# Kernel tuning notes

Hardware: AMD Instinct MI355X
Metric: run time of the kernel (lower is better)

Reference implementation:

```python
import jax, jax.numpy as jnp
import numpy as np
import math

B, S, D = 2, 2048, 2048
H = 16
HD = D // H          # 128
LAT = 512            # latent_dim


def setup_inputs() -> dict:
    key = jax.random.key(0)
    ks = jax.random.split(key, 8)
    x = jax.random.normal(ks[0], (B, S, D), dtype=jnp.float32)
    freqs = jax.random.uniform(ks[1], (S, HD // 2), dtype=jnp.float32) * (2 * math.pi)
    # additive causal mask: 0 on/below diagonal, -1e9 above
    causal = jnp.tril(jnp.ones((S, S), dtype=bool))
    mask = jnp.where(causal, 0.0, -1e9).astype(jnp.float32)
    sc = 0.02
    Wq = jax.random.normal(ks[2], (D, H * HD), dtype=jnp.float32) * sc
    Wdown = jax.random.normal(ks[3], (D, LAT), dtype=jnp.float32) * sc
    Wkup = jax.random.normal(ks[4], (LAT, H * HD), dtype=jnp.float32) * sc
    Wvup = jax.random.normal(ks[5], (LAT, H * HD), dtype=jnp.float32) * sc
    Wo = jax.random.normal(ks[6], (D, D), dtype=jnp.float32) * sc
    return {"x": x, "freqs": freqs, "mask": mask,
            "Wq": Wq, "Wdown": Wdown, "Wkup": Wkup, "Wvup": Wvup, "Wo": Wo}


def _apply_rope(t, cos, sin):
    # t: [B, S, H, HD]; cos/sin: [1, S, 1, HD//2]
    tp = t.reshape(t.shape[:-1] + (HD // 2, 2))
    t0, t1 = tp[..., 0], tp[..., 1]
    rot = jnp.stack([t0 * cos - t1 * sin, t0 * sin + t1 * cos], axis=-1)
    return rot.reshape(t.shape)


def reference(x, freqs, mask, Wq, Wdown, Wkup, Wvup, Wo):
    b, s, d = x.shape
    Q = (x @ Wq).reshape(b, s, H, HD)
    c_kv = x @ Wdown                       # [B, S, LAT] low-rank latent
    K = (c_kv @ Wkup).reshape(b, s, H, HD)
    V = (c_kv @ Wvup).reshape(b, s, H, HD)
    cos = jnp.cos(freqs)[None, :, None, :]
    sin = jnp.sin(freqs)[None, :, None, :]
    Q = _apply_rope(Q, cos, sin)
    K = _apply_rope(K, cos, sin)
    scores = jnp.einsum('bqhd,bkhd->bhqk', Q, K) / math.sqrt(HD)
    scores = scores + mask                 # [S,S] broadcast over [B,H,S,S]
    probs = jax.nn.softmax(scores, axis=-1)
    attn = jnp.einsum('bhqk,bkhd->bqhd', probs, V).reshape(b, s, d)
    return attn @ Wo
```

## Files before the change

### kernel.cpp

```cpp
#include <hip/hip_runtime.h>
#include <hip/hip_bf16.h>
#include <math.h>

typedef __hip_bfloat16 bf16;
typedef __attribute__((ext_vector_type(8))) short short8;
typedef __attribute__((ext_vector_type(4))) float f32x4;
typedef __attribute__((ext_vector_type(16))) float f32x16;

static constexpr int BB   = 2;
static constexpr int SS   = 2048;
static constexpr int DD   = 2048;
static constexpr int NH   = 16;
static constexpr int HDD  = 128;
static constexpr int LATD = 512;
static constexpr int MR   = BB * SS;
static constexpr int QRS  = DD + LATD;

#if __has_builtin(__builtin_amdgcn_exp2f)
#define EXP2F(x) __builtin_amdgcn_exp2f(x)
#else
#define EXP2F(x) exp2f(x)
#endif

__device__ __forceinline__ void async_cp16(const void* g, void* l) {
    __builtin_amdgcn_global_load_lds(
        (const __attribute__((address_space(1))) void*)g,
        (__attribute__((address_space(3))) void*)l, 16, 0, 0);
}

__device__ __forceinline__ unsigned short bf_bits(bf16 v) {
    union { bf16 b; unsigned short u; } cv; cv.b = v; return cv.u;
}

__global__ __launch_bounds__(256) void prep(
    const float* __restrict__ x, bf16* __restrict__ xb,
    const float* __restrict__ Wq, const float* __restrict__ Wdown,
    const float* __restrict__ Wkup, const float* __restrict__ Wvup,
    bf16* __restrict__ WqdT, bf16* __restrict__ WkvT) {
    __shared__ float tile[32][33];
    const int blk = blockIdx.x, tid = threadIdx.x;
    if (blk < 8192) {
        const int i = blk * 256 + tid;
        float4 v = ((const float4*)x)[i];
        ushort4 o;
        o.x = bf_bits(__float2bfloat16(v.x));
        o.y = bf_bits(__float2bfloat16(v.y));
        o.z = bf_bits(__float2bfloat16(v.z));
        o.w = bf_bits(__float2bfloat16(v.w));
        ((ushort4*)xb)[i] = o;
        return;
    }
    const float* in; bf16* out; int rows, cols, bx, by;
    if (blk < 12288) {
        const int l = blk - 8192;  in = Wq;    out = WqdT;
        rows = DD;   cols = DD;    bx = l & 63; by = l >> 6;
    } else if (blk < 13312) {
        const int l = blk - 12288; in = Wdown; out = WqdT + (size_t)DD * DD;
        rows = DD;   cols = LATD;  bx = l & 15; by = l >> 4;
    } else if (blk < 14336) {
        const int l = blk - 13312; in = Wkup;  out = WkvT;
        rows = LATD; cols = DD;    bx = l & 63; by = l >> 6;
    } else {
        const int l = blk - 14336; in = Wvup;  out = WkvT + (size_t)DD * LATD;
        rows = LATD; cols = DD;    bx = l & 63; by = l >> 6;
    }
    const int tx = tid & 31, ty = tid >> 5;
    const int c0 = bx * 32, r0 = by * 32;
    for (int i = 0; i < 32; i += 8)
        tile[ty + i][tx] = in[(size_t)(r0 + ty + i) * cols + c0 + tx];
    __syncthreads();
    for (int i = 0; i < 32; i += 8)
        out[(size_t)(c0 + ty + i) * rows + r0 + tx] =
            __float2bfloat16(tile[tx][ty + i]);
}

template <bool OUT_F32>
__global__ __launch_bounds__(256) void gemm_bt(
    const bf16* __restrict__ A, const bf16* __restrict__ Bt,
    void* __restrict__ Cout, int M, int N, int K, int lda, int ldb, int ldc) {
    __shared__ bf16 As[2][128 * 32];
    __shared__ bf16 Bs[2][128 * 32];
    const int tid  = threadIdx.x;
    const int lane = tid & 63, wave = tid >> 6;
    const int quad = lane >> 4, l16 = lane & 15;
    const int row0 = blockIdx.y * 128, col0 = blockIdx.x * 128;
    const int wm = (wave >> 1) * 64, wn = (wave & 1) * 64;
    const int srow = lane >> 2;
    const int scol = (lane & 3) * 8;

    f32x4 acc[4][4];
    for (int i = 0; i < 4; ++i)
        for (int j = 0; j < 4; ++j)
            for (int r = 0; r < 4; ++r) acc[i][j][r] = 0.f;

    auto stage = [&](int k0, int bufi) {
        for (int c = 0; c < 2; ++c) {
            const int chunk = wave * 2 + c;
            const int r = chunk * 16 + srow;
            async_cp16(A  + (size_t)(row0 + r) * lda + k0 + scol, &As[bufi][chunk * 512]);
            async_cp16(Bt + (size_t)(col0 + r) * ldb + k0 + scol, &Bs[bufi][chunk * 512]);
        }
    };

    const int nk = K / 32;
    stage(0, 0);
    for (int ki = 0; ki < nk; ++ki) {
        __syncthreads();
        if (ki + 1 < nk) stage((ki + 1) * 32, (ki + 1) & 1);
        const int bi = ki & 1;
        short8 af[4], bfr[4];
        for (int t = 0; t < 4; ++t) {
            af[t]  = *(const short8*)&As[bi][(wm + t * 16 + l16) * 32 + quad * 8];
            bfr[t] = *(const short8*)&Bs[bi][(wn + t * 16 + l16) * 32 + quad * 8];
        }
        for (int i = 0; i < 4; ++i)
            for (int j = 0; j < 4; ++j)
                acc[i][j] = __builtin_amdgcn_mfma_f32_16x16x32_bf16(
                    af[i], bfr[j], acc[i][j], 0, 0, 0);
    }

    const int rbase = row0 + wm + quad * 4;
    const int cbase = col0 + wn + l16;
    if (OUT_F32) {
        float* C = (float*)Cout;
        for (int i = 0; i < 4; ++i)
            for (int j = 0; j < 4; ++j)
                for (int r = 0; r < 4; ++r)
                    C[(size_t)(rbase + i * 16 + r) * ldc + cbase + j * 16] = acc[i][j][r];
    } else {
        bf16* C = (bf16*)Cout;
        for (int i = 0; i < 4; ++i)
            for (int j = 0; j < 4; ++j)
                for (int r = 0; r < 4; ++r)
                    C[(size_t)(rbase + i * 16 + r) * ldc + cbase + j * 16] =
                        __float2bfloat16(acc[i][j][r]);
    }
}

__global__ __launch_bounds__(256) void tvrope(
    bf16* __restrict__ KV, bf16* __restrict__ VT,
    const float* __restrict__ freqs,
    const float* __restrict__ Wo, bf16* __restrict__ WoT) {
    __shared__ __align__(16) char sm[64 * 74 * 2];
    const int blk = blockIdx.x, tid = threadIdx.x;
    if (blk < 2048) {
        bf16 (*t)[74] = (bf16(*)[74])sm;
        const int bx = blk & 31, byy = (blk >> 5) & 1, bh = blk >> 6;
        const int s0 = bx * 64, d0 = byy * 64;
        const int b = bh >> 4, h = bh & 15;
        const bf16* src = KV + (size_t)b * SS * 4096 + 2048 + h * 128 + d0;
        for (int p = 0; p < 2; ++p) {
            const int s = p * 32 + (tid >> 3), dc = (tid & 7) * 8;
            short8 v = *(const short8*)(src + (size_t)(s0 + s) * 4096 + dc);
            const bf16* ve = (const bf16*)&v;
            for (int e = 0; e < 8; ++e) t[s][dc + e] = ve[e];
        }
        __syncthreads();
        bf16* dst = VT + ((size_t)bh * HDD + d0) * SS + s0;
        for (int p = 0; p < 2; ++p) {
            const int d = p * 32 + (tid >> 3), g = tid & 7;
            short8 v; bf16* ve = (bf16*)&v;
            for (int e = 0; e < 8; ++e) ve[e] = t[g * 8 + e][d];
            const int gp = g ^ (d & 7);
            *(short8*)(dst + (size_t)d * SS + gp * 8) = v;
        }
        return;
    }
    if (blk < 6144) {
        const int idx = (blk - 2048) * 256 + tid;
        const int pg  = idx & 15;
        const int h   = (idx >> 4) & (NH - 1);
        const int tok = idx >> 8;
        const int s   = tok & (SS - 1);
        const float4 f = *(const float4*)&freqs[s * 64 + pg * 4];
        const float fr[4] = {f.x, f.y, f.z, f.w};
        bf16* kp = KV + (size_t)tok * 4096 + h * HDD + pg * 8;
        short8 v = *(const short8*)kp;
        const bf16* ve = (const bf16*)&v;
        short8 o; bf16* oe = (bf16*)&o;
        for (int i = 0; i < 4; ++i) {
            const float cs = __cosf(fr[i]), sn = __sinf(fr[i]);
            const float t0 = __bfloat162float(ve[2 * i]);
            const float t1 = __bfloat162float(ve[2 * i + 1]);
            oe[2 * i]     = __float2bfloat16(t0 * cs - t1 * sn);
            oe[2 * i + 1] = __float2bfloat16(t0 * sn + t1 * cs);
        }
        *(short8*)kp = o;
        return;
    }
    {
        float (*tile)[33] = (float(*)[33])sm;
        const int l = blk - 6144;
        const int bx = l & 63, by = l >> 6;
        const int tx = tid & 31, ty = tid >> 5;
        const int c0 = bx * 32, r0 = by * 32;
        for (int i = 0; i < 32; i += 8)
            tile[ty + i][tx] = Wo[(size_t)(r0 + ty + i) * DD + c0 + tx];
        __syncthreads();
        for (int i = 0; i < 32; i += 8)
            WoT[(size_t)(c0 + ty + i) * DD + r0 + tx] =
                __float2bfloat16(tile[tx][ty + i]);
    }
}

__global__ __launch_bounds__(256, 2) void flash_attn(
    const bf16* __restrict__ QC, const bf16* __restrict__ KV,
    const bf16* __restrict__ VTg, const float* __restrict__ freqs,
    bf16* __restrict__ O) {
    const int j = blockIdx.x;
    const int bh = (j >> 3) & 31, q3 = j & 7;
    const int qt = (j & 256) ? q3 : 15 - q3;
    const int h = bh & (NH - 1), b = bh >> 4;
    const int q0 = qt * 128;
    const int tid = threadIdx.x, lane = tid & 63, wave = tid >> 6;
    const int l32 = lane & 31, hi = lane >> 5;

    __shared__ __align__(16) char smem[66048];
    bf16*  KsB  = (bf16*)smem;
    bf16*  VtB  = (bf16*)(smem + 32768);
    float* RedS = (float*)(smem + 65536);

    const bf16* Kb  = KV  + (size_t)b * SS * 4096 + h * HDD;
    const bf16* VTb = VTg + (size_t)bh * HDD * SS;

    const float QS = 0.08838834764831845f * 1.4426950408889634f;
    const int qrow = q0 + wave * 32 + l32;
    short8 qf[8];
    {
        const bf16* qp = QC + (size_t)(b * SS + qrow) * QRS + h * HDD;
#pragma unroll
        for (int dk = 0; dk < 8; ++dk) {
            short8 v = *(const short8*)(qp + dk * 16 + hi * 8);
            const float4 f = *(const float4*)&freqs[(size_t)qrow * 64 + dk * 8 + hi * 4];
            const float fr[4] = {f.x, f.y, f.z, f.w};
            const bf16* ve = (const bf16*)&v;
            bf16* oe = (bf16*)&qf[dk];
#pragma unroll
            for (int i2 = 0; i2 < 4; ++i2) {
                const float cs = __cosf(fr[i2]), sn = __sinf(fr[i2]);
                const float t0 = __bfloat162float(ve[2 * i2]);
                const float t1 = __bfloat162float(ve[2 * i2 + 1]);
                oe[2 * i2]     = __float2bfloat16((t0 * cs - t1 * sn) * QS);
                oe[2 * i2 + 1] = __float2bfloat16((t0 * sn + t1 * cs) * QS);
            }
        }
    }

    auto stage = [&](int kt, int bufi) {
        const int k0 = kt * 64;
#pragma unroll
        for (int ii = 0; ii < 4; ++ii) {
            const int i = wave * 4 + ii;
            const int krow = 4 * i + (lane >> 4);
            const int csrc = (lane & 15) ^ (krow & 7);
            async_cp16(Kb + (size_t)(k0 + krow) * 4096 + csrc * 8,
                       KsB + bufi * 8192 + i * 512);
            const int d = 8 * i + (lane >> 3);
            async_cp16(VTb + (size_t)d * SS + k0 + (lane & 7) * 8,
                       VtB + bufi * 8192 + i * 512);
        }
    };

    f32x16 accO[4];
#pragma unroll
    for (int d = 0; d < 4; ++d)
#pragma unroll
        for (int r = 0; r < 16; ++r) accO[d][r] = 0.f;
    float m_r = -1e30f, l_r = 0.f;

    const int ktMax = 2 * qt + 1;
    const int qwb = q0 + wave * 32;

    stage(0, 0);
    for (int kt = 0; kt <= ktMax; ++kt) {
        const int k0 = kt * 64;
        __syncthreads();
        if (kt < ktMax) stage(kt + 1, (kt + 1) & 1);
        const int bi = kt & 1;

        if (k0 > qwb + 31) continue;

        f32x16 st[2];
#pragma unroll
        for (int t = 0; t < 2; ++t)
#pragma unroll
            for (int r = 0; r < 16; ++r) st[t][r] = 0.f;
        __builtin_amdgcn_s_setprio(1);
#pragma unroll
        for (int dk = 0; dk < 8; ++dk)
#pragma unroll
            for (int t = 0; t < 2; ++t) {
                const int rd = t * 32 + l32;
                short8 kf = *(const short8*)
                    &KsB[bi * 8192 + rd * 128 + ((((dk << 1) | hi) ^ (rd & 7)) << 3)];
                st[t] = __builtin_amdgcn_mfma_f32_32x32x16_bf16(
                    kf, qf[dk], st[t], 0, 0, 0);
            }
        __builtin_amdgcn_s_setprio(0);

        float p[32];
#pragma unroll
        for (int t = 0; t < 2; ++t)
#pragma unroll
            for (int r = 0; r < 16; ++r) p[t * 16 + r] = st[t][r];

        if (k0 + 63 > qwb) {
#pragma unroll
            for (int t = 0; t < 2; ++t)
#pragma unroll
                for (int r = 0; r < 16; ++r) {
                    const int kv = k0 + t * 32 + (r & 3) + 8 * (r >> 2) + 4 * hi;
                    if (kv > qrow) p[t * 16 + r] = -1e30f;
                }
        }

        float mt[16];
#pragma unroll
        for (int n = 0; n < 16; ++n) mt[n] = fmaxf(p[n], p[n + 16]);
#pragma unroll
        for (int n = 0; n < 8; ++n) mt[n] = fmaxf(mt[n], mt[n + 8]);
#pragma unroll
        for (int n = 0; n < 4; ++n) mt[n] = fmaxf(mt[n], mt[n + 4]);
        float mx = fmaxf(fmaxf(mt[0], mt[1]), fmaxf(mt[2], mt[3]));
        const float rmax = fmaxf(mx, __shfl_xor(mx, 32));

        const bool grow = rmax > m_r + 8.f;
        if (__any(grow)) {
            const float mnew = fmaxf(m_r, rmax);
            const float alpha = EXP2F(m_r - mnew);
            m_r = mnew;
            l_r *= alpha;
            RedS[wave * 32 + l32] = alpha;
            __builtin_amdgcn_s_waitcnt(0xc07f);
#pragma unroll
            for (int r = 0; r < 16; ++r) {
                const float av = RedS[wave * 32 + ((r & 3) + 8 * (r >> 2) + 4 * hi)];
#pragma unroll
                for (int d = 0; d < 4; ++d) accO[d][r] *= av;
            }
        }

#pragma unroll
        for (int r = 0; r < 32; ++r) p[r] = EXP2F(p[r] - m_r);
        float sa[16];
#pragma unroll
        for (int n = 0; n < 16; ++n) sa[n] = p[n] + p[n + 16];
#pragma unroll
        for (int n = 0; n < 8; ++n) sa[n] += sa[n + 8];
#pragma unroll
        for (int n = 0; n < 4; ++n) sa[n] += sa[n + 4];
        float ps = (sa[0] + sa[1]) + (sa[2] + sa[3]);
        l_r += ps + __shfl_xor(ps, 32);

        unsigned int pk[16];
#pragma unroll
        for (int n = 0; n < 16; ++n) {
            const unsigned int lo = bf_bits(__float2bfloat16(p[2 * n]));
            const unsigned int hl = bf_bits(__float2bfloat16(p[2 * n + 1]));
            pk[n] = lo | (hl << 16);
        }

#pragma unroll
        for (int m = 0; m < 4; ++m) {
            const int A0 = 4 * m;
            const unsigned int op0 = __shfl_xor(pk[A0 + 0], 32);
            const unsigned int op1 = __shfl_xor(pk[A0 + 1], 32);
            const unsigned int op2 = __shfl_xor(pk[A0 + 2], 32);
            const unsigned int op3 = __shfl_xor(pk[A0 + 3], 32);
            union { unsigned int w[4]; short8 s; } fr;
            fr.w[0] = hi ? op2 : pk[A0 + 0];
            fr.w[1] = hi ? op3 : pk[A0 + 1];
            fr.w[2] = hi ? pk[A0 + 2] : op0;
            fr.w[3] = hi ? pk[A0 + 3] : op1;
            __builtin_amdgcn_s_setprio(1);
#pragma unroll
            for (int db = 0; db < 4; ++db) {
                const int d = db * 32 + l32;
                short8 vf = *(const short8*)
                    &VtB[bi * 8192 + d * 64 + ((((m << 1) | hi) ^ (d & 7)) << 3)];
                accO[db] = __builtin_amdgcn_mfma_f32_32x32x16_bf16(
                    fr.s, vf, accO[db], 0, 0, 0);
            }
            __builtin_amdgcn_s_setprio(0);
        }
    }

    const float invl = 1.f / l_r;
    RedS[wave * 32 + l32] = invl;
    __builtin_amdgcn_s_waitcnt(0xc07f);
    bf16* Ob = O + (size_t)b * SS * DD + h * HDD;
#pragma unroll
    for (int r = 0; r < 16; ++r) {
        const int row = (r & 3) + 8 * (r >> 2) + 4 * hi;
        const float iv = RedS[wave * 32 + row];
        const size_t ro = (size_t)(q0 + wave * 32 + row) * DD;
#pragma unroll
        for (int db = 0; db < 4; ++db)
            Ob[ro + db * 32 + l32] = __float2bfloat16(accO[db][r] * iv);
    }
}

extern "C" void kernel_launch(void* const* d_in, const int* in_sizes, int n_in,
                              void* d_out, int out_size, void* d_ws, size_t ws_size,
                              hipStream_t stream) {
    (void)in_sizes; (void)n_in; (void)out_size; (void)ws_size;
    const float* x     = (const float*)d_in[0];
    const float* freqs = (const float*)d_in[1];
    const float* Wq    = (const float*)d_in[3];
    const float* Wdown = (const float*)d_in[4];
    const float* Wkup  = (const float*)d_in[5];
    const float* Wvup  = (const float*)d_in[6];
    const float* Wo    = (const float*)d_in[7];
    float* out = (float*)d_out;

    char* ws = (char*)d_ws;
    size_t off = 0;
    auto take = [&](size_t bytes) -> void* {
        void* p = ws + off;
        off += (bytes + 255) & ~(size_t)255;
        return p;
    };
    bf16* xb    = (bf16*)take((size_t)MR * DD * 2);
    bf16* WqdT  = (bf16*)take((size_t)QRS * DD * 2);
    bf16* WkvT  = (bf16*)take((size_t)2 * DD * LATD * 2);
    bf16* QC    = (bf16*)take((size_t)MR * QRS * 2);
    bf16* KVb   = (bf16*)take((size_t)MR * 2 * DD * 2);
    bf16* VTg   = (bf16*)take((size_t)BB * NH * HDD * SS * 2);
    bf16* attn  = xb;
    bf16* WoT   = WqdT;

    prep<<<15360, 256, 0, stream>>>(x, xb, Wq, Wdown, Wkup, Wvup, WqdT, WkvT);

    gemm_bt<false><<<dim3(QRS / 128, MR / 128), 256, 0, stream>>>(
        xb, WqdT, QC, MR, QRS, DD, DD, DD, QRS);
    gemm_bt<false><<<dim3(2 * DD / 128, MR / 128), 256, 0, stream>>>(
        QC + DD, WkvT, KVb, MR, 2 * DD, LATD, QRS, LATD, 2 * DD);

    tvrope<<<10240, 256, 0, stream>>>(KVb, VTg, freqs, Wo, WoT);

    flash_attn<<<512, 256, 0, stream>>>(QC, KVb, VTg, freqs, attn);

    gemm_bt<true><<<dim3(DD / 128, MR / 128), 256, 0, stream>>>(
        attn, WoT, out, MR, DD, DD, DD, DD, DD);
}
```

Before: 347.3 us.

## Process two 32-row query sub-tiles per wave with 128-thread attention blocks

The flash attention kernel now runs 2 waves per block instead of 4, and each wave handles 64 query rows as two 32-row sub-tiles. Every K and V fragment read from LDS feeds two MFMAs, which halves LDS reads per FLOP. Each wave also issues twice as many staging copies. In exchange register pressure roughly doubles for accumulators and Q fragments, launch bounds drop to one block of 128 threads, and there are fewer waves per CU to hide latency. The causal early-exit is now coarser (64-row granularity), so some masked work is computed.

Measured after the change: 423.9 us. +22.0%, slower.

```diff
diff --git a/kernel.cpp b/kernel.cpp
--- a/kernel.cpp
+++ b/kernel.cpp
@@ -203,7 +203,7 @@
     }
 }
 
-__global__ __launch_bounds__(256, 2) void flash_attn(
+__global__ __launch_bounds__(128, 1) void flash_attn(
     const bf16* __restrict__ QC, const bf16* __restrict__ KV,
     const bf16* __restrict__ VTg, const float* __restrict__ freqs,
     bf16* __restrict__ O) {
@@ -224,17 +224,19 @@
     const bf16* VTb = VTg + (size_t)bh * HDD * SS;
 
     const float QS = 0.08838834764831845f * 1.4426950408889634f;
-    const int qrow = q0 + wave * 32 + l32;
-    short8 qf[8];
-    {
-        const bf16* qp = QC + (size_t)(b * SS + qrow) * QRS + h * HDD;
+    const int qwb = q0 + wave * 64;
+    short8 qf[2][8];
+#pragma unroll
+    for (int s = 0; s < 2; ++s) {
+        const int qr = qwb + s * 32 + l32;
+        const bf16* qp = QC + (size_t)(b * SS + qr) * QRS + h * HDD;
 #pragma unroll
         for (int dk = 0; dk < 8; ++dk) {
             short8 v = *(const short8*)(qp + dk * 16 + hi * 8);
-            const float4 f = *(const float4*)&freqs[(size_t)qrow * 64 + dk * 8 + hi * 4];
+            const float4 f = *(const float4*)&freqs[(size_t)qr * 64 + dk * 8 + hi * 4];
             const float fr[4] = {f.x, f.y, f.z, f.w};
             const bf16* ve = (const bf16*)&v;
-            bf16* oe = (bf16*)&qf[dk];
+            bf16* oe = (bf16*)&qf[s][dk];
 #pragma unroll
             for (int i2 = 0; i2 < 4; ++i2) {
                 const float cs = __cosf(fr[i2]), sn = __sinf(fr[i2]);
@@ -249,8 +251,8 @@
     auto stage = [&](int kt, int bufi) {
         const int k0 = kt * 64;
 #pragma unroll
-        for (int ii = 0; ii < 4; ++ii) {
-            const int i = wave * 4 + ii;
+        for (int ii = 0; ii < 8; ++ii) {
+            const int i = wave * 8 + ii;
             const int krow = 4 * i + (lane >> 4);
             const int csrc = (lane & 15) ^ (krow & 7);
             async_cp16(Kb + (size_t)(k0 + krow) * 4096 + csrc * 8,
@@ -261,15 +263,16 @@
         }
     };
 
-    f32x16 accO[4];
-#pragma unroll
-    for (int d = 0; d < 4; ++d)
-#pragma unroll
-        for (int r = 0; r < 16; ++r) accO[d][r] = 0.f;
-    float m_r = -1e30f, l_r = 0.f;
+    f32x16 accO[2][4];
+#pragma unroll
+    for (int s = 0; s < 2; ++s)
+#pragma unroll
+        for (int d = 0; d < 4; ++d)
+#pragma unroll
+            for (int r = 0; r < 16; ++r) accO[s][d][r] = 0.f;
+    float m_r[2] = {-1e30f, -1e30f}, l_r[2] = {0.f, 0.f};
 
     const int ktMax = 2 * qt + 1;
-    const int qwb = q0 + wave * 32;
 
     stage(0, 0);
     for (int kt = 0; kt <= ktMax; ++kt) {
@@ -278,13 +281,15 @@
         if (kt < ktMax) stage(kt + 1, (kt + 1) & 1);
         const int bi = kt & 1;
 
-        if (k0 > qwb + 31) continue;
-
-        f32x16 st[2];
-#pragma unroll
-        for (int t = 0; t < 2; ++t)
-#pragma unroll
-            for (int r = 0; r < 16; ++r) st[t][r] = 0.f;
+        if (k0 > qwb + 63) continue;
+
+        f32x16 st[2][2];
+#pragma unroll
+        for (int s = 0; s < 2; ++s)
+#pragma unroll
+            for (int t = 0; t < 2; ++t)
+#pragma unroll
+                for (int r = 0; r < 16; ++r) st[s][t][r] = 0.f;
         __builtin_amdgcn_s_setprio(1);
 #pragma unroll
         for (int dk = 0; dk < 8; ++dk)
@@ -293,111 +298,126 @@
                 const int rd = t * 32 + l32;
                 short8 kf = *(const short8*)
                     &KsB[bi * 8192 + rd * 128 + ((((dk << 1) | hi) ^ (rd & 7)) << 3)];
-                st[t] = __builtin_amdgcn_mfma_f32_32x32x16_bf16(
-                    kf, qf[dk], st[t], 0, 0, 0);
+                st[0][t] = __builtin_amdgcn_mfma_f32_32x32x16_bf16(
+                    kf, qf[0][dk], st[0][t], 0, 0, 0);
+                st[1][t] = __builtin_amdgcn_mfma_f32_32x32x16_bf16(
+                    kf, qf[1][dk], st[1][t], 0, 0, 0);
             }
         __builtin_amdgcn_s_setprio(0);
 
-        float p[32];
-#pragma unroll
-        for (int t = 0; t < 2; ++t)
-#pragma unroll
-            for (int r = 0; r < 16; ++r) p[t * 16 + r] = st[t][r];
-
-        if (k0 + 63 > qwb) {
+        unsigned int pk[2][16];
+        const bool boundary = (k0 + 63 > qwb);
+#pragma unroll
+        for (int s = 0; s < 2; ++s) {
+            float p[32];
 #pragma unroll
             for (int t = 0; t < 2; ++t)
 #pragma unroll
+                for (int r = 0; r < 16; ++r) p[t * 16 + r] = st[s][t][r];
+
+            if (boundary) {
+                const int qr = qwb + s * 32 + l32;
+#pragma unroll
+                for (int t = 0; t < 2; ++t)
+#pragma unroll
+                    for (int r = 0; r < 16; ++r) {
+                        const int kv = k0 + t * 32 + (r & 3) + 8 * (r >> 2) + 4 * hi;
+                        if (kv > qr) p[t * 16 + r] = -1e30f;
+                    }
+            }
+
+            float mt[16];
+#pragma unroll
+            for (int n = 0; n < 16; ++n) mt[n] = fmaxf(p[n], p[n + 16]);
+#pragma unroll
+            for (int n = 0; n < 8; ++n) mt[n] = fmaxf(mt[n], mt[n + 8]);
+#pragma unroll
+            for (int n = 0; n < 4; ++n) mt[n] = fmaxf(mt[n], mt[n + 4]);
+            float mx = fmaxf(fmaxf(mt[0], mt[1]), fmaxf(mt[2], mt[3]));
+            const float rmax = fmaxf(mx, __shfl_xor(mx, 32));
+
+            const bool grow = rmax > m_r[s] + 8.f;
+            if (__any(grow)) {
+                const float mnew = fmaxf(m_r[s], rmax);
+                const float alpha = EXP2F(m_r[s] - mnew);
+                m_r[s] = mnew;
+                l_r[s] *= alpha;
+                RedS[(wave * 2 + s) * 32 + l32] = alpha;
+                __builtin_amdgcn_s_waitcnt(0xc07f);
+#pragma unroll
                 for (int r = 0; r < 16; ++r) {
-                    const int kv = k0 + t * 32 + (r & 3) + 8 * (r >> 2) + 4 * hi;
-                    if (kv > qrow) p[t * 16 + r] = -1e30f;
+                    const float av =
+                        RedS[(wave * 2 + s) * 32 + ((r & 3) + 8 * (r >> 2) + 4 * hi)];
+#pragma unroll
+                    for (int d = 0; d < 4; ++d) accO[s][d][r] *= av;
                 }
-        }
-
-        float mt[16];
-#pragma unroll
-        for (int n = 0; n < 16; ++n) mt[n] = fmaxf(p[n], p[n + 16]);
-#pragma unroll
-        for (int n = 0; n < 8; ++n) mt[n] = fmaxf(mt[n], mt[n + 8]);
-#pragma unroll
-        for (int n = 0; n < 4; ++n) mt[n] = fmaxf(mt[n], mt[n + 4]);
-        float mx = fmaxf(fmaxf(mt[0], mt[1]), fmaxf(mt[2], mt[3]));
-        const float rmax = fmaxf(mx, __shfl_xor(mx, 32));
-
-        const bool grow = rmax > m_r + 8.f;
-        if (__any(grow)) {
-            const float mnew = fmaxf(m_r, rmax);
-            const float alpha = EXP2F(m_r - mnew);
-            m_r = mnew;
-            l_r *= alpha;
-            RedS[wave * 32 + l32] = alpha;
-            __builtin_amdgcn_s_waitcnt(0xc07f);
-#pragma unroll
-            for (int r = 0; r < 16; ++r) {
-                const float av = RedS[wave * 32 + ((r & 3) + 8 * (r >> 2) + 4 * hi)];
-#pragma unroll
-                for (int d = 0; d < 4; ++d) accO[d][r] *= av;
-            }
-        }
-
-#pragma unroll
-        for (int r = 0; r < 32; ++r) p[r] = EXP2F(p[r] - m_r);
-        float sa[16];
-#pragma unroll
-        for (int n = 0; n < 16; ++n) sa[n] = p[n] + p[n + 16];
-#pragma unroll
-        for (int n = 0; n < 8; ++n) sa[n] += sa[n + 8];
-#pragma unroll
-        for (int n = 0; n < 4; ++n) sa[n] += sa[n + 4];
-        float ps = (sa[0] + sa[1]) + (sa[2] + sa[3]);
-        l_r += ps + __shfl_xor(ps, 32);
-
-        unsigned int pk[16];
-#pragma unroll
-        for (int n = 0; n < 16; ++n) {
-            const unsigned int lo = bf_bits(__float2bfloat16(p[2 * n]));
-            const unsigned int hl = bf_bits(__float2bfloat16(p[2 * n + 1]));
-            pk[n] = lo | (hl << 16);
+            }
+
+#pragma unroll
+            for (int r = 0; r < 32; ++r) p[r] = EXP2F(p[r] - m_r[s]);
+            float sa[16];
+#pragma unroll
+            for (int n = 0; n < 16; ++n) sa[n] = p[n] + p[n + 16];
+#pragma unroll
+            for (int n = 0; n < 8; ++n) sa[n] += sa[n + 8];
+#pragma unroll
+            for (int n = 0; n < 4; ++n) sa[n] += sa[n + 4];
+            float ps = (sa[0] + sa[1]) + (sa[2] + sa[3]);
+            l_r[s] += ps + __shfl_xor(ps, 32);
+
+#pragma unroll
+            for (int n = 0; n < 16; ++n) {
+                const unsigned int lo = bf_bits(__float2bfloat16(p[2 * n]));
+                const unsigned int hl = bf_bits(__float2bfloat16(p[2 * n + 1]));
+                pk[s][n] = lo | (hl << 16);
+            }
         }
 
 #pragma unroll
         for (int m = 0; m < 4; ++m) {
             const int A0 = 4 * m;
-            const unsigned int op0 = __shfl_xor(pk[A0 + 0], 32);
-            const unsigned int op1 = __shfl_xor(pk[A0 + 1], 32);
-            const unsigned int op2 = __shfl_xor(pk[A0 + 2], 32);
-            const unsigned int op3 = __shfl_xor(pk[A0 + 3], 32);
-            union { unsigned int w[4]; short8 s; } fr;
-            fr.w[0] = hi ? op2 : pk[A0 + 0];
-            fr.w[1] = hi ? op3 : pk[A0 + 1];
-            fr.w[2] = hi ? pk[A0 + 2] : op0;
-            fr.w[3] = hi ? pk[A0 + 3] : op1;
+            union { unsigned int w[4]; short8 s8; } fr[2];
+#pragma unroll
+            for (int s = 0; s < 2; ++s) {
+                const unsigned int u = hi ? pk[s][A0 + 0] : pk[s][A0 + 2];
+                const unsigned int v = hi ? pk[s][A0 + 1] : pk[s][A0 + 3];
+                const unsigned int su = __shfl_xor(u, 32);
+                const unsigned int sv = __shfl_xor(v, 32);
+                fr[s].w[0] = hi ? su : pk[s][A0 + 0];
+                fr[s].w[1] = hi ? sv : pk[s][A0 + 1];
+                fr[s].w[2] = hi ? pk[s][A0 + 2] : su;
+                fr[s].w[3] = hi ? pk[s][A0 + 3] : sv;
+            }
             __builtin_amdgcn_s_setprio(1);
 #pragma unroll
             for (int db = 0; db < 4; ++db) {
                 const int d = db * 32 + l32;
                 short8 vf = *(const short8*)
                     &VtB[bi * 8192 + d * 64 + ((((m << 1) | hi) ^ (d & 7)) << 3)];
-                accO[db] = __builtin_amdgcn_mfma_f32_32x32x16_bf16(
-                    fr.s, vf, accO[db], 0, 0, 0);
+                accO[0][db] = __builtin_amdgcn_mfma_f32_32x32x16_bf16(
+                    fr[0].s8, vf, accO[0][db], 0, 0, 0);
+                accO[1][db] = __builtin_amdgcn_mfma_f32_32x32x16_bf16(
+                    fr[1].s8, vf, accO[1][db], 0, 0, 0);
             }
             __builtin_amdgcn_s_setprio(0);
         }
     }
 
-    const float invl = 1.f / l_r;
-    RedS[wave * 32 + l32] = invl;
+    RedS[(wave * 2 + 0) * 32 + l32] = 1.f / l_r[0];
+    RedS[(wave * 2 + 1) * 32 + l32] = 1.f / l_r[1];
     __builtin_amdgcn_s_waitcnt(0xc07f);
     bf16* Ob = O + (size_t)b * SS * DD + h * HDD;
 #pragma unroll
-    for (int r = 0; r < 16; ++r) {
-        const int row = (r & 3) + 8 * (r >> 2) + 4 * hi;
-        const float iv = RedS[wave * 32 + row];
-        const size_t ro = (size_t)(q0 + wave * 32 + row) * DD;
-#pragma unroll
-        for (int db = 0; db < 4; ++db)
-            Ob[ro + db * 32 + l32] = __float2bfloat16(accO[db][r] * iv);
-    }
+    for (int s = 0; s < 2; ++s)
+#pragma unroll
+        for (int r = 0; r < 16; ++r) {
+            const int row = (r & 3) + 8 * (r >> 2) + 4 * hi;
+            const float iv = RedS[(wave * 2 + s) * 32 + row];
+            const size_t ro = (size_t)(qwb + s * 32 + row) * DD;
+#pragma unroll
+            for (int db = 0; db < 4; ++db)
+                Ob[ro + db * 32 + l32] = __float2bfloat16(accO[s][db][r] * iv);
+        }
 }
 
 extern "C" void kernel_launch(void* const* d_in, const int* in_sizes, int n_in,
@@ -438,7 +458,7 @@
 
     tvrope<<<10240, 256, 0, stream>>>(KVb, VTg, freqs, Wo, WoT);
 
-    flash_attn<<<512, 256, 0, stream>>>(QC, KVb, VTg, freqs, attn);
+    flash_attn<<<512, 128, 0, stream>>>(QC, KVb, VTg, freqs, attn);
 
     gemm_bt<true><<<dim3(DD / 128, MR / 128), 256, 0, stream>>>(
         attn, WoT, out, MR, DD, DD, DD, DD, DD);
```

## Replace GEMM with 256x256-tile, 4-stage pipelined, swizzled LDS kernel

Applied to the files above, without the earlier changes.

Swaps the 128x128 double-buffered GEMM for a 512-thread kernel computing 256x256 output tiles with a 4-deep async-copy ring buffer in 128KB of LDS. It XOR-swizzles LDS columns to avoid bank conflicts, remaps workgroup IDs into banded tiles for L2 locality, and splits each k-step into two MFMA halves with s_setprio around loads. The aim is more data reuse per byte loaded and better overlap of memory with MFMA. In exchange each CU holds one workgroup, so small grids (e.g. 160 or 256 blocks on 256 CUs) may leave the machine underfilled.

Result: slower. 366.3 us (+5.5%).

```diff
diff --git a/kernel.cpp b/kernel.cpp
--- a/kernel.cpp
+++ b/kernel.cpp
@@ -75,65 +75,120 @@
 }
 
 template <bool OUT_F32>
-__global__ __launch_bounds__(256) void gemm_bt(
+__global__ __launch_bounds__(512) void gemm256(
     const bf16* __restrict__ A, const bf16* __restrict__ Bt,
     void* __restrict__ Cout, int M, int N, int K, int lda, int ldb, int ldc) {
-    __shared__ bf16 As[2][128 * 32];
-    __shared__ bf16 Bs[2][128 * 32];
+    __shared__ __align__(16) char smem[131072];
     const int tid  = threadIdx.x;
     const int lane = tid & 63, wave = tid >> 6;
     const int quad = lane >> 4, l16 = lane & 15;
-    const int row0 = blockIdx.y * 128, col0 = blockIdx.x * 128;
-    const int wm = (wave >> 1) * 64, wn = (wave & 1) * 64;
-    const int srow = lane >> 2;
-    const int scol = (lane & 3) * 8;
-
-    f32x4 acc[4][4];
-    for (int i = 0; i < 4; ++i)
-        for (int j = 0; j < 4; ++j)
-            for (int r = 0; r < 4; ++r) acc[i][j][r] = 0.f;
-
-    auto stage = [&](int k0, int bufi) {
-        for (int c = 0; c < 2; ++c) {
-            const int chunk = wave * 2 + c;
-            const int r = chunk * 16 + srow;
-            async_cp16(A  + (size_t)(row0 + r) * lda + k0 + scol, &As[bufi][chunk * 512]);
-            async_cp16(Bt + (size_t)(col0 + r) * ldb + k0 + scol, &Bs[bufi][chunk * 512]);
-        }
+    const int wm = wave >> 2, wn = wave & 3;
+
+    const int nx = N >> 8, ny = M >> 8;
+    const int nwg = nx * ny;
+    const int wg   = ((blockIdx.x & 7) * (nwg >> 3)) + (blockIdx.x >> 3);
+    const int idx  = wg % (nx << 2);
+    const int band = wg / (nx << 2);
+    const int bcol = idx >> 2, brow = (band << 2) + (idx & 3);
+    const int row0 = brow << 8, col0 = bcol << 8;
+
+    const int NT = K >> 5;
+
+    auto stageL = [&](int tile, int l) {
+        char* ldst = smem + (size_t)((tile & 3) * 32768 + l * 8192) + tid * 16;
+        const int rr = l * 128 + (tid >> 2);
+        const int sc = (tid & 3) ^ (rr & 3);
+        if (l < 2)
+            async_cp16(A + (size_t)(row0 + rr) * lda + tile * 32 + sc * 8, ldst);
+        else
+            async_cp16(Bt + (size_t)(col0 + (rr - 256)) * ldb + tile * 32 + sc * 8, ldst);
     };
 
-    const int nk = K / 32;
-    stage(0, 0);
-    for (int ki = 0; ki < nk; ++ki) {
-        __syncthreads();
-        if (ki + 1 < nk) stage((ki + 1) * 32, (ki + 1) & 1);
-        const int bi = ki & 1;
-        short8 af[4], bfr[4];
-        for (int t = 0; t < 4; ++t) {
-            af[t]  = *(const short8*)&As[bi][(wm + t * 16 + l16) * 32 + quad * 8];
-            bfr[t] = *(const short8*)&Bs[bi][(wn + t * 16 + l16) * 32 + quad * 8];
-        }
-        for (int i = 0; i < 4; ++i)
-            for (int j = 0; j < 4; ++j)
-                acc[i][j] = __builtin_amdgcn_mfma_f32_16x16x32_bf16(
-                    af[i], bfr[j], acc[i][j], 0, 0, 0);
-    }
-
-    const int rbase = row0 + wm + quad * 4;
-    const int cbase = col0 + wn + l16;
+    f32x4 acc[8][4];
+#pragma unroll
+    for (int m = 0; m < 8; ++m)
+#pragma unroll
+        for (int n = 0; n < 4; ++n)
+#pragma unroll
+            for (int r = 0; r < 4; ++r) acc[m][n][r] = 0.f;
+
+    for (int tt = 0; tt < 3; ++tt)
+#pragma unroll
+        for (int l = 0; l < 4; ++l) stageL(tt, l);
+    asm volatile("s_waitcnt vmcnt(8)" ::: "memory");
+    __builtin_amdgcn_s_barrier();
+
+    for (int t = 0; t < NT; ++t) {
+        const char* base = smem + (size_t)(t & 3) * 32768;
+        const bool more = (t + 3) < NT;
+
+        short8 bfr[4], afA[4];
+#pragma unroll
+        for (int n = 0; n < 4; ++n) {
+            const int row = wn * 64 + n * 16 + l16;
+            bfr[n] = *(const short8*)(base + 16384 + row * 64 + ((quad ^ (row & 3)) << 4));
+        }
+#pragma unroll
+        for (int m = 0; m < 4; ++m) {
+            const int row = wm * 128 + m * 16 + l16;
+            afA[m] = *(const short8*)(base + row * 64 + ((quad ^ (row & 3)) << 4));
+        }
+        if (more) { stageL(t + 3, 0); stageL(t + 3, 1); }
+        __builtin_amdgcn_s_barrier();
+        __builtin_amdgcn_s_waitcnt(0xc07f);
+        __builtin_amdgcn_s_setprio(1);
+#pragma unroll
+        for (int m = 0; m < 4; ++m)
+#pragma unroll
+            for (int n = 0; n < 4; ++n)
+                acc[m][n] = __builtin_amdgcn_mfma_f32_16x16x32_bf16(
+                    afA[m], bfr[n], acc[m][n], 0, 0, 0);
+        __builtin_amdgcn_s_setprio(0);
+        __builtin_amdgcn_s_barrier();
+
+        short8 afB[4];
+#pragma unroll
+        for (int m = 0; m < 4; ++m) {
+            const int row = wm * 128 + (m + 4) * 16 + l16;
+            afB[m] = *(const short8*)(base + row * 64 + ((quad ^ (row & 3)) << 4));
+        }
+        if (more) { stageL(t + 3, 2); stageL(t + 3, 3); }
+        if (more) asm volatile("s_waitcnt vmcnt(8)" ::: "memory");
+        else      asm volatile("s_waitcnt vmcnt(0)" ::: "memory");
+        __builtin_amdgcn_s_barrier();
+        __builtin_amdgcn_s_waitcnt(0xc07f);
+        __builtin_amdgcn_s_setprio(1);
+#pragma unroll
+        for (int m = 0; m < 4; ++m)
+#pragma unroll
+            for (int n = 0; n < 4; ++n)
+                acc[m + 4][n] = __builtin_amdgcn_mfma_f32_16x16x32_bf16(
+                    afB[m], bfr[n], acc[m + 4][n], 0, 0, 0);
+        __builtin_amdgcn_s_setprio(0);
+        __builtin_amdgcn_s_barrier();
+    }
+
+    const int rbase = row0 + wm * 128 + quad * 4;
+    const int cbase = col0 + wn * 64 + l16;
     if (OUT_F32) {
         float* C = (float*)Cout;
-        for (int i = 0; i < 4; ++i)
-            for (int j = 0; j < 4; ++j)
+#pragma unroll
+        for (int m = 0; m < 8; ++m)
+#pragma unroll
+            for (int n = 0; n < 4; ++n)
+#pragma unroll
                 for (int r = 0; r < 4; ++r)
-                    C[(size_t)(rbase + i * 16 + r) * ldc + cbase + j * 16] = acc[i][j][r];
+                    C[(size_t)(rbase + m * 16 + r) * ldc + cbase + n * 16] = acc[m][n][r];
     } else {
         bf16* C = (bf16*)Cout;
-        for (int i = 0; i < 4; ++i)
-            for (int j = 0; j < 4; ++j)
+#pragma unroll
+        for (int m = 0; m < 8; ++m)
+#pragma unroll
+            for (int n = 0; n < 4; ++n)
+#pragma unroll
                 for (int r = 0; r < 4; ++r)
-                    C[(size_t)(rbase + i * 16 + r) * ldc + cbase + j * 16] =
-                        __float2bfloat16(acc[i][j][r]);
+                    C[(size_t)(rbase + m * 16 + r) * ldc + cbase + n * 16] =
+                        __float2bfloat16(acc[m][n][r]);
     }
 }
 
@@ -431,15 +486,15 @@
 
     prep<<<15360, 256, 0, stream>>>(x, xb, Wq, Wdown, Wkup, Wvup, WqdT, WkvT);
 
-    gemm_bt<false><<<dim3(QRS / 128, MR / 128), 256, 0, stream>>>(
+    gemm256<false><<<(QRS / 256) * (MR / 256), 512, 0, stream>>>(
         xb, WqdT, QC, MR, QRS, DD, DD, DD, QRS);
-    gemm_bt<false><<<dim3(2 * DD / 128, MR / 128), 256, 0, stream>>>(
+    gemm256<false><<<(2 * DD / 256) * (MR / 256), 512, 0, stream>>>(
         QC + DD, WkvT, KVb, MR, 2 * DD, LATD, QRS, LATD, 2 * DD);
 
     tvrope<<<10240, 256, 0, stream>>>(KVb, VTg, freqs, Wo, WoT);
 
     flash_attn<<<512, 256, 0, stream>>>(QC, KVb, VTg, freqs, attn);
 
-    gemm_bt<true><<<dim3(DD / 128, MR / 128), 256, 0, stream>>>(
+    gemm256<true><<<(DD / 256) * (MR / 256), 512, 0, stream>>>(
         attn, WoT, out, MR, DD, DD, DD, DD, DD);
 }
```
